# Performance work log

Hardware: AMD Instinct MI355X
Metric: run time of the kernel (lower is better)

The kernel has to match this reference:

```python
import jax, jax.numpy as jnp
import numpy as np

N, M_CTX, SIN, YDIM, SPROJ = 16384, 4096, 256, 7, 256


def setup_inputs() -> dict:
    key = jax.random.key(0)
    k1, k2, k3, k4, k5 = jax.random.split(key, 5)
    return {
        "x": jax.random.normal(k1, (N, SIN), dtype=jnp.float32),
        "y": jax.random.normal(k2, (M_CTX, YDIM), dtype=jnp.float32),
        "Wq": jax.random.normal(k3, (SIN, SPROJ), dtype=jnp.float32) / np.sqrt(SIN),
        "Wk": jax.random.normal(k4, (YDIM, SPROJ), dtype=jnp.float32) / np.sqrt(YDIM),
        "Wv": jax.random.normal(k5, (YDIM, SPROJ), dtype=jnp.float32) / np.sqrt(YDIM),
    }


def smooth_softmax(x):
    # softmax over keys (axis=1) blended with 0.1*relu, renormalized
    s = jax.nn.softmax(x, axis=1)
    num = jax.nn.relu(x) * 0.1 + s
    return num / jnp.sum(num, axis=1, keepdims=True)


def reference(x, y, Wq, Wk, Wv):
    XQ = x @ Wq            # [N, P]
    YK = y @ Wk            # [M, P]
    YV = y @ Wv            # [M, P]
    scores = (XQ @ YK.T) / jnp.sqrt(jnp.asarray(YK.shape[1], XQ.dtype))  # [N, M]
    A = smooth_softmax(scores)
    return A @ YV          # [N, P]
```

## Files before the change

### kernel.cpp

```cpp
#include <hip/hip_runtime.h>
#include <hip/hip_bf16.h>

#define N_Q   16384
#define MCTX  4096
#define DSIN  256
#define YDIM  7
#define PDIM  256
#define BK    32

typedef __attribute__((ext_vector_type(8))) short s16x8;
typedef __attribute__((ext_vector_type(4))) float f32x4;
typedef unsigned short u16;

static __device__ __forceinline__ u16 f2bf(float f) {
    union { float f; unsigned u; } v; v.f = f;
    unsigned r = v.u + 0x7fffu + ((v.u >> 16) & 1u);
    return (u16)(r >> 16);
}
static __device__ __forceinline__ float bf2f(u16 h) {
    union { unsigned u; float f; } v; v.u = ((unsigned)h) << 16;
    return v.f;
}
static __device__ __forceinline__ f32x4 mfma16(s16x8 a, s16x8 b, f32x4 c) {
    return __builtin_amdgcn_mfma_f32_16x16x32_bf16(a, b, c, 0, 0, 0);
}
static __device__ __forceinline__ void gload_lds16(const u16* g, u16* l) {
    __builtin_amdgcn_global_load_lds(
        (const __attribute__((address_space(1))) unsigned int*)(g),
        (__attribute__((address_space(3))) unsigned int*)(l), 16, 0, 0);
}

__global__ void k_wt(const float* __restrict__ Wq, u16* __restrict__ WtH,
                     u16* __restrict__ WtL) {
    int n = blockIdx.x;
    int k = threadIdx.x;
    float w = Wq[(size_t)k * PDIM + n];
    u16 h = f2bf(w);
    WtH[(size_t)n * DSIN + k] = h;
    WtL[(size_t)n * DSIN + k] = f2bf(w - bf2f(h));
}

__global__ void k_ykv(const float* __restrict__ y, const float* __restrict__ Wk,
                      const float* __restrict__ Wv, u16* __restrict__ YK,
                      u16* __restrict__ YVb) {
    int kb = blockIdx.x;
    int p  = threadIdx.x;
    float wk[YDIM], wv[YDIM];
#pragma unroll
    for (int j = 0; j < YDIM; ++j) {
        wk[j] = Wk[(size_t)j * PDIM + p];
        wv[j] = Wv[(size_t)j * PDIM + p];
    }
    u16 vbuf[32];
#pragma unroll
    for (int m = 0; m < 32; ++m) {
        int key = kb * 32 + m;
        float ak = 0.f, av = 0.f;
#pragma unroll
        for (int j = 0; j < YDIM; ++j) {
            float yy = y[(size_t)key * YDIM + j];
            ak += yy * wk[j];
            av += yy * wv[j];
        }
        YK[(size_t)key * PDIM + p] = f2bf(ak * 0.0625f);
        vbuf[m] = f2bf(av);
    }
    s16x8* dst = (s16x8*)(YVb + ((size_t)kb * PDIM + p) * 32);
#pragma unroll
    for (int c = 0; c < 4; ++c) dst[c] = ((s16x8*)vbuf)[c];
}

__global__ __launch_bounds__(256, 1) void k_xq(const float* __restrict__ x,
                                               const u16* __restrict__ WtH,
                                               const u16* __restrict__ WtL,
                                               u16* __restrict__ XQ) {
    __shared__ u16 xH[64 * 256];
    __shared__ u16 xL[64 * 256];
    const int tid = threadIdx.x;
    const int rowg0 = blockIdx.x * 64;

#pragma unroll
    for (int i = 0; i < 8; ++i) {
        int row = (tid >> 5) + i * 8;
        int c32 = tid & 31;
        const float* px = x + (size_t)(rowg0 + row) * DSIN + c32 * 8;
        float4 a = *(const float4*)px;
        float4 b = *(const float4*)(px + 4);
        float vals[8] = {a.x, a.y, a.z, a.w, b.x, b.y, b.z, b.w};
        s16x8 h, l;
#pragma unroll
        for (int j = 0; j < 8; ++j) {
            u16 hh = f2bf(vals[j]);
            h[j] = (short)hh;
            l[j] = (short)f2bf(vals[j] - bf2f(hh));
        }
        int pc = c32 ^ (row & 7);
        *(s16x8*)(xH + row * 256 + pc * 8) = h;
        *(s16x8*)(xL + row * 256 + pc * 8) = l;
    }
    __syncthreads();

    const int wave = tid >> 6, lane = tid & 63;
    const int quad = lane >> 4, m16 = lane & 15;
    const int rowl = wave * 16 + m16;
    const int swz = rowl & 7;
    s16x8 ah[8], al[8];
#pragma unroll
    for (int kf = 0; kf < 8; ++kf) {
        int pc = (kf * 4 + quad) ^ swz;
        ah[kf] = *(const s16x8*)(xH + rowl * 256 + pc * 8);
        al[kf] = *(const s16x8*)(xL + rowl * 256 + pc * 8);
    }
#pragma unroll
    for (int pt = 0; pt < 16; ++pt) {
        f32x4 acc = (f32x4){0.f, 0.f, 0.f, 0.f};
#pragma unroll
        for (int kf = 0; kf < 8; ++kf) {
            size_t idx = (size_t)(pt * 16 + m16) * DSIN + kf * 32 + quad * 8;
            s16x8 bh = *(const s16x8*)(WtH + idx);
            s16x8 bl = *(const s16x8*)(WtL + idx);
            acc = mfma16(ah[kf], bh, acc);
            acc = mfma16(al[kf], bh, acc);
            acc = mfma16(ah[kf], bl, acc);
        }
#pragma unroll
        for (int r = 0; r < 4; ++r)
            XQ[(size_t)(rowg0 + wave * 16 + quad * 4 + r) * PDIM + pt * 16 + m16] =
                f2bf(acc[r]);
    }
}

__global__ __launch_bounds__(256, 2) void k_attn(const u16* __restrict__ XQ,
                                                 const u16* __restrict__ YK,
                                                 const u16* __restrict__ YVb,
                                                 float* __restrict__ accE,
                                                 float* __restrict__ accR,
                                                 float* __restrict__ lsum,
                                                 float* __restrict__ rsum,
                                                 int msPerSplit) {
    __shared__ u16 Kt[32 * 256];
    __shared__ u16 Pe[64 * 40];
    __shared__ u16 Pr[64 * 40];

    const int tid = threadIdx.x;
    const int wave = tid >> 6, lane = tid & 63;
    const int quad = lane >> 4, m16 = lane & 15;
    const int split = blockIdx.y;
    const int qbase = blockIdx.x * 64;
    const int key_begin = split * msPerSplit;
    const int iters = msPerSplit / BK;
    const int pslice = wave * 64;
    const int swz = m16 & 7;

    s16x8 qf[8];
    const u16* qp = XQ + (size_t)(qbase + wave * 16 + m16) * DSIN;
#pragma unroll
    for (int kf = 0; kf < 8; ++kf)
        qf[kf] = *(const s16x8*)(qp + kf * 32 + quad * 8);

    f32x4 aE[4][4], aR[4][4];
#pragma unroll
    for (int g = 0; g < 4; ++g)
#pragma unroll
        for (int t = 0; t < 4; ++t) {
            aE[g][t] = (f32x4){0.f, 0.f, 0.f, 0.f};
            aR[g][t] = (f32x4){0.f, 0.f, 0.f, 0.f};
        }
    float lacc[4] = {0.f, 0.f, 0.f, 0.f}, racc[4] = {0.f, 0.f, 0.f, 0.f};

    auto stage = [&](int key0) {
#pragma unroll
        for (int c = 0; c < 4; ++c) {
            int l = (wave * 4 + c) * 64 + lane;
            int r = l >> 5;
            int sc = (l & 31) ^ (r & 7);
            gload_lds16(YK + (size_t)(key0 + r) * DSIN + sc * 8,
                        Kt + (size_t)(wave * 4 + c) * 512);
        }
    };
    stage(key_begin);

    for (int it = 0; it < iters; ++it) {
        const int key0 = key_begin + it * BK;
        __syncthreads();

        f32x4 s0 = (f32x4){0.f, 0.f, 0.f, 0.f};
        f32x4 s1 = (f32x4){0.f, 0.f, 0.f, 0.f};
#pragma unroll
        for (int kf = 0; kf < 8; ++kf) {
            int pc = (kf * 4 + quad) ^ swz;
            s16x8 b0 = *(const s16x8*)(Kt + m16 * 256 + pc * 8);
            s16x8 b1 = *(const s16x8*)(Kt + (16 + m16) * 256 + pc * 8);
            s0 = mfma16(qf[kf], b0, s0);
            s1 = mfma16(qf[kf], b1, s1);
        }
#pragma unroll
        for (int r = 0; r < 4; ++r) {
            float e0 = __expf(s0[r]), e1 = __expf(s1[r]);
            float rl0 = fmaxf(s0[r], 0.f), rl1 = fmaxf(s1[r], 0.f);
            lacc[r] += e0 + e1;
            racc[r] += rl0 + rl1;
            int row = wave * 16 + quad * 4 + r;
            Pe[row * 40 + m16]      = f2bf(e0);
            Pe[row * 40 + 16 + m16] = f2bf(e1);
            Pr[row * 40 + m16]      = f2bf(rl0);
            Pr[row * 40 + 16 + m16] = f2bf(rl1);
        }
        __syncthreads();

        s16x8 vf[4];
        const u16* vb = YVb + (size_t)((key0 >> 5) * PDIM) * 32;
#pragma unroll
        for (int t = 0; t < 4; ++t)
            vf[t] = *(const s16x8*)(vb + (size_t)(pslice + t * 16 + m16) * 32 + quad * 8);

        if (it + 1 < iters) stage(key0 + BK);

#pragma unroll
        for (int g = 0; g < 4; ++g) {
            s16x8 pa = *(const s16x8*)(Pe + (g * 16 + m16) * 40 + quad * 8);
            s16x8 pb = *(const s16x8*)(Pr + (g * 16 + m16) * 40 + quad * 8);
#pragma unroll
            for (int t = 0; t < 4; ++t) {
                aE[g][t] = mfma16(pa, vf[t], aE[g][t]);
                aR[g][t] = mfma16(pb, vf[t], aR[g][t]);
            }
        }
    }

    size_t ob = ((size_t)split * N_Q + qbase) * PDIM;
#pragma unroll
    for (int g = 0; g < 4; ++g)
#pragma unroll
        for (int t = 0; t < 4; ++t)
#pragma unroll
            for (int r = 0; r < 4; ++r) {
                size_t o = ob + (size_t)(g * 16 + quad * 4 + r) * PDIM + pslice + t * 16 + m16;
                accE[o] = aE[g][t][r];
                accR[o] = aR[g][t][r];
            }
#pragma unroll
    for (int r = 0; r < 4; ++r) {
        lacc[r] += __shfl_xor(lacc[r], 1);
        lacc[r] += __shfl_xor(lacc[r], 2);
        lacc[r] += __shfl_xor(lacc[r], 4);
        lacc[r] += __shfl_xor(lacc[r], 8);
        racc[r] += __shfl_xor(racc[r], 1);
        racc[r] += __shfl_xor(racc[r], 2);
        racc[r] += __shfl_xor(racc[r], 4);
        racc[r] += __shfl_xor(racc[r], 8);
    }
    if (m16 < 4) {
        float lv = (m16 == 0) ? lacc[0] : (m16 == 1) ? lacc[1] : (m16 == 2) ? lacc[2] : lacc[3];
        float rv = (m16 == 0) ? racc[0] : (m16 == 1) ? racc[1] : (m16 == 2) ? racc[2] : racc[3];
        int row = split * N_Q + qbase + wave * 16 + quad * 4 + m16;
        lsum[row] = lv;
        rsum[row] = rv;
    }
}

__global__ void k_comb(const float* __restrict__ accE, const float* __restrict__ accR,
                       const float* __restrict__ lsum, const float* __restrict__ rsum,
                       float* __restrict__ out, int nsplit) {
    int row = blockIdx.x * 4 + (threadIdx.x >> 6);
    size_t idx = (size_t)row * PDIM + (threadIdx.x & 63) * 4;
    const size_t NP = (size_t)N_Q * PDIM;
    float4 E = {0.f, 0.f, 0.f, 0.f}, R = {0.f, 0.f, 0.f, 0.f};
    float L = 0.f, Rs = 0.f;
    for (int s = 0; s < nsplit; ++s) {
        float4 e = *(const float4*)(accE + s * NP + idx);
        float4 r = *(const float4*)(accR + s * NP + idx);
        E.x += e.x; E.y += e.y; E.z += e.z; E.w += e.w;
        R.x += r.x; R.y += r.y; R.z += r.z; R.w += r.w;
        L  += lsum[(size_t)s * N_Q + row];
        Rs += rsum[(size_t)s * N_Q + row];
    }
    float invL = 1.f / L, invD = 1.f / (1.f + 0.1f * Rs);
    float4 o;
    o.x = (0.1f * R.x + E.x * invL) * invD;
    o.y = (0.1f * R.y + E.y * invL) * invD;
    o.z = (0.1f * R.z + E.z * invL) * invD;
    o.w = (0.1f * R.w + E.w * invL) * invD;
    *(float4*)(out + idx) = o;
}

extern "C" void kernel_launch(void* const* d_in, const int* in_sizes, int n_in,
                              void* d_out, int out_size, void* d_ws, size_t ws_size,
                              hipStream_t stream) {
    const float* x  = (const float*)d_in[0];
    const float* y  = (const float*)d_in[1];
    const float* Wq = (const float*)d_in[2];
    const float* Wk = (const float*)d_in[3];
    const float* Wv = (const float*)d_in[4];
    float* out = (float*)d_out;

    char* ws = (char*)d_ws;
    size_t off = 0;
    auto take = [&](size_t bytes) -> char* {
        char* p = ws + off;
        off += (bytes + 255) & ~(size_t)255;
        return p;
    };
    u16* XQ  = (u16*)take((size_t)N_Q * PDIM * 2);
    u16* WtH = (u16*)take((size_t)PDIM * DSIN * 2);
    u16* WtL = (u16*)take((size_t)PDIM * DSIN * 2);
    u16* YK  = (u16*)take((size_t)MCTX * PDIM * 2);
    u16* YVb = (u16*)take((size_t)MCTX * PDIM * 2);

    size_t perSplit = (size_t)N_Q * PDIM * 4 * 2 + (size_t)N_Q * 4 * 2 + 1024;
    int nsplit = (ws_size >= off + 2 * perSplit + 4096) ? 2 : 1;

    float* accE = (float*)take((size_t)nsplit * N_Q * PDIM * 4);
    float* accR = (float*)take((size_t)nsplit * N_Q * PDIM * 4);
    float* lsum = (float*)take((size_t)nsplit * N_Q * 4);
    float* rsum = (float*)take((size_t)nsplit * N_Q * 4);

    hipLaunchKernelGGL(k_wt,   dim3(PDIM),     dim3(DSIN), 0, stream, Wq, WtH, WtL);
    hipLaunchKernelGGL(k_ykv,  dim3(MCTX/32),  dim3(PDIM), 0, stream, y, Wk, Wv, YK, YVb);
    hipLaunchKernelGGL(k_xq,   dim3(N_Q/64),   dim3(256),  0, stream, x, WtH, WtL, XQ);
    hipLaunchKernelGGL(k_attn, dim3(N_Q/64, nsplit), dim3(256), 0, stream,
                       XQ, YK, YVb, accE, accR, lsum, rsum, MCTX / nsplit);
    hipLaunchKernelGGL(k_comb, dim3(N_Q/4),    dim3(256),  0, stream,
                       accE, accR, lsum, rsum, out, nsplit);
}
```

Measured before the change: 236.6 us.

## Shrink query tiles, split keys across waves, store bf16 partials, add setprio

Halves the query tile in k_xq and k_attn from 64 to 32 rows. In k_attn each wave now computes scores for one 16-key half of the block and the row sums are reduced through shared memory; occupancy hints are raised. The split-K partial accumulators are stored as bf16 instead of fp32, halving the write and read traffic in k_comb, at some cost in precision. s_setprio is wrapped around the MFMA sections to favour matrix issue. The smaller tile doubles the number of YK/YV loads per query row, trading reuse for parallelism and occupancy.

```diff
diff --git a/kernel.cpp b/kernel.cpp
--- a/kernel.cpp
+++ b/kernel.cpp
@@ -70,17 +70,17 @@
     for (int c = 0; c < 4; ++c) dst[c] = ((s16x8*)vbuf)[c];
 }
 
-__global__ __launch_bounds__(256, 1) void k_xq(const float* __restrict__ x,
+__global__ __launch_bounds__(256, 2) void k_xq(const float* __restrict__ x,
                                                const u16* __restrict__ WtH,
                                                const u16* __restrict__ WtL,
                                                u16* __restrict__ XQ) {
-    __shared__ u16 xH[64 * 256];
-    __shared__ u16 xL[64 * 256];
+    __shared__ u16 xH[32 * 256];
+    __shared__ u16 xL[32 * 256];
     const int tid = threadIdx.x;
-    const int rowg0 = blockIdx.x * 64;
-
-#pragma unroll
-    for (int i = 0; i < 8; ++i) {
+    const int rowg0 = blockIdx.x * 32;
+
+#pragma unroll
+    for (int i = 0; i < 4; ++i) {
         int row = (tid >> 5) + i * 8;
         int c32 = tid & 31;
         const float* px = x + (size_t)(rowg0 + row) * DSIN + c32 * 8;
@@ -102,7 +102,8 @@
 
     const int wave = tid >> 6, lane = tid & 63;
     const int quad = lane >> 4, m16 = lane & 15;
-    const int rowl = wave * 16 + m16;
+    const int rh = wave & 1, ph = wave >> 1;
+    const int rowl = rh * 16 + m16;
     const int swz = rowl & 7;
     s16x8 ah[8], al[8];
 #pragma unroll
@@ -112,7 +113,8 @@
         al[kf] = *(const s16x8*)(xL + rowl * 256 + pc * 8);
     }
 #pragma unroll
-    for (int pt = 0; pt < 16; ++pt) {
+    for (int ptl = 0; ptl < 8; ++ptl) {
+        int pt = ph * 8 + ptl;
         f32x4 acc = (f32x4){0.f, 0.f, 0.f, 0.f};
 #pragma unroll
         for (int kf = 0; kf < 8; ++kf) {
@@ -125,42 +127,45 @@
         }
 #pragma unroll
         for (int r = 0; r < 4; ++r)
-            XQ[(size_t)(rowg0 + wave * 16 + quad * 4 + r) * PDIM + pt * 16 + m16] =
+            XQ[(size_t)(rowg0 + rh * 16 + quad * 4 + r) * PDIM + pt * 16 + m16] =
                 f2bf(acc[r]);
     }
 }
 
-__global__ __launch_bounds__(256, 2) void k_attn(const u16* __restrict__ XQ,
+__global__ __launch_bounds__(256, 3) void k_attn(const u16* __restrict__ XQ,
                                                  const u16* __restrict__ YK,
                                                  const u16* __restrict__ YVb,
-                                                 float* __restrict__ accE,
-                                                 float* __restrict__ accR,
+                                                 u16* __restrict__ accE,
+                                                 u16* __restrict__ accR,
                                                  float* __restrict__ lsum,
                                                  float* __restrict__ rsum,
                                                  int msPerSplit) {
     __shared__ u16 Kt[32 * 256];
-    __shared__ u16 Pe[64 * 40];
-    __shared__ u16 Pr[64 * 40];
+    __shared__ u16 Pe[32 * 40];
+    __shared__ u16 Pr[32 * 40];
+    __shared__ float Lred[2][32];
+    __shared__ float Rred[2][32];
 
     const int tid = threadIdx.x;
     const int wave = tid >> 6, lane = tid & 63;
     const int quad = lane >> 4, m16 = lane & 15;
+    const int rh = wave >> 1, kh = wave & 1;
     const int split = blockIdx.y;
-    const int qbase = blockIdx.x * 64;
+    const int qbase = blockIdx.x * 32;
     const int key_begin = split * msPerSplit;
     const int iters = msPerSplit / BK;
     const int pslice = wave * 64;
     const int swz = m16 & 7;
 
     s16x8 qf[8];
-    const u16* qp = XQ + (size_t)(qbase + wave * 16 + m16) * DSIN;
+    const u16* qp = XQ + (size_t)(qbase + rh * 16 + m16) * DSIN;
 #pragma unroll
     for (int kf = 0; kf < 8; ++kf)
         qf[kf] = *(const s16x8*)(qp + kf * 32 + quad * 8);
 
-    f32x4 aE[4][4], aR[4][4];
-#pragma unroll
-    for (int g = 0; g < 4; ++g)
+    f32x4 aE[2][4], aR[2][4];
+#pragma unroll
+    for (int g = 0; g < 2; ++g)
 #pragma unroll
         for (int t = 0; t < 4; ++t) {
             aE[g][t] = (f32x4){0.f, 0.f, 0.f, 0.f};
@@ -185,26 +190,23 @@
         __syncthreads();
 
         f32x4 s0 = (f32x4){0.f, 0.f, 0.f, 0.f};
-        f32x4 s1 = (f32x4){0.f, 0.f, 0.f, 0.f};
+        __builtin_amdgcn_s_setprio(1);
 #pragma unroll
         for (int kf = 0; kf < 8; ++kf) {
             int pc = (kf * 4 + quad) ^ swz;
-            s16x8 b0 = *(const s16x8*)(Kt + m16 * 256 + pc * 8);
-            s16x8 b1 = *(const s16x8*)(Kt + (16 + m16) * 256 + pc * 8);
+            s16x8 b0 = *(const s16x8*)(Kt + (kh * 16 + m16) * 256 + pc * 8);
             s0 = mfma16(qf[kf], b0, s0);
-            s1 = mfma16(qf[kf], b1, s1);
-        }
+        }
+        __builtin_amdgcn_s_setprio(0);
 #pragma unroll
         for (int r = 0; r < 4; ++r) {
-            float e0 = __expf(s0[r]), e1 = __expf(s1[r]);
-            float rl0 = fmaxf(s0[r], 0.f), rl1 = fmaxf(s1[r], 0.f);
-            lacc[r] += e0 + e1;
-            racc[r] += rl0 + rl1;
-            int row = wave * 16 + quad * 4 + r;
-            Pe[row * 40 + m16]      = f2bf(e0);
-            Pe[row * 40 + 16 + m16] = f2bf(e1);
-            Pr[row * 40 + m16]      = f2bf(rl0);
-            Pr[row * 40 + 16 + m16] = f2bf(rl1);
+            float e0 = __expf(s0[r]);
+            float rl0 = fmaxf(s0[r], 0.f);
+            lacc[r] += e0;
+            racc[r] += rl0;
+            int row = rh * 16 + quad * 4 + r;
+            Pe[row * 40 + kh * 16 + m16] = f2bf(e0);
+            Pr[row * 40 + kh * 16 + m16] = f2bf(rl0);
         }
         __syncthreads();
 
@@ -216,8 +218,9 @@
 
         if (it + 1 < iters) stage(key0 + BK);
 
-#pragma unroll
-        for (int g = 0; g < 4; ++g) {
+        __builtin_amdgcn_s_setprio(1);
+#pragma unroll
+        for (int g = 0; g < 2; ++g) {
             s16x8 pa = *(const s16x8*)(Pe + (g * 16 + m16) * 40 + quad * 8);
             s16x8 pb = *(const s16x8*)(Pr + (g * 16 + m16) * 40 + quad * 8);
 #pragma unroll
@@ -226,18 +229,19 @@
                 aR[g][t] = mfma16(pb, vf[t], aR[g][t]);
             }
         }
+        __builtin_amdgcn_s_setprio(0);
     }
 
     size_t ob = ((size_t)split * N_Q + qbase) * PDIM;
 #pragma unroll
-    for (int g = 0; g < 4; ++g)
+    for (int g = 0; g < 2; ++g)
 #pragma unroll
         for (int t = 0; t < 4; ++t)
 #pragma unroll
             for (int r = 0; r < 4; ++r) {
                 size_t o = ob + (size_t)(g * 16 + quad * 4 + r) * PDIM + pslice + t * 16 + m16;
-                accE[o] = aE[g][t][r];
-                accR[o] = aR[g][t][r];
+                accE[o] = f2bf(aE[g][t][r]);
+                accR[o] = f2bf(aR[g][t][r]);
             }
 #pragma unroll
     for (int r = 0; r < 4; ++r) {
@@ -250,38 +254,54 @@
         racc[r] += __shfl_xor(racc[r], 4);
         racc[r] += __shfl_xor(racc[r], 8);
     }
-    if (m16 < 4) {
-        float lv = (m16 == 0) ? lacc[0] : (m16 == 1) ? lacc[1] : (m16 == 2) ? lacc[2] : lacc[3];
-        float rv = (m16 == 0) ? racc[0] : (m16 == 1) ? racc[1] : (m16 == 2) ? racc[2] : racc[3];
-        int row = split * N_Q + qbase + wave * 16 + quad * 4 + m16;
-        lsum[row] = lv;
-        rsum[row] = rv;
-    }
-}
-
-__global__ void k_comb(const float* __restrict__ accE, const float* __restrict__ accR,
+    if (m16 == 0) {
+#pragma unroll
+        for (int r = 0; r < 4; ++r) {
+            Lred[kh][rh * 16 + quad * 4 + r] = lacc[r];
+            Rred[kh][rh * 16 + quad * 4 + r] = racc[r];
+        }
+    }
+    __syncthreads();
+    if (tid < 32) {
+        int row = split * N_Q + qbase + tid;
+        lsum[row] = Lred[0][tid] + Lred[1][tid];
+        rsum[row] = Rred[0][tid] + Rred[1][tid];
+    }
+}
+
+__global__ void k_comb(const u16* __restrict__ accE, const u16* __restrict__ accR,
                        const float* __restrict__ lsum, const float* __restrict__ rsum,
                        float* __restrict__ out, int nsplit) {
-    int row = blockIdx.x * 4 + (threadIdx.x >> 6);
-    size_t idx = (size_t)row * PDIM + (threadIdx.x & 63) * 4;
+    int row = blockIdx.x * 8 + (threadIdx.x >> 5);
+    int col = (threadIdx.x & 31) * 8;
+    size_t idx = (size_t)row * PDIM + col;
     const size_t NP = (size_t)N_Q * PDIM;
-    float4 E = {0.f, 0.f, 0.f, 0.f}, R = {0.f, 0.f, 0.f, 0.f};
+    float E[8] = {0.f, 0.f, 0.f, 0.f, 0.f, 0.f, 0.f, 0.f};
+    float R[8] = {0.f, 0.f, 0.f, 0.f, 0.f, 0.f, 0.f, 0.f};
     float L = 0.f, Rs = 0.f;
     for (int s = 0; s < nsplit; ++s) {
-        float4 e = *(const float4*)(accE + s * NP + idx);
-        float4 r = *(const float4*)(accR + s * NP + idx);
-        E.x += e.x; E.y += e.y; E.z += e.z; E.w += e.w;
-        R.x += r.x; R.y += r.y; R.z += r.z; R.w += r.w;
+        s16x8 e = *(const s16x8*)(accE + s * NP + idx);
+        s16x8 r = *(const s16x8*)(accR + s * NP + idx);
+#pragma unroll
+        for (int j = 0; j < 8; ++j) {
+            E[j] += bf2f((u16)e[j]);
+            R[j] += bf2f((u16)r[j]);
+        }
         L  += lsum[(size_t)s * N_Q + row];
         Rs += rsum[(size_t)s * N_Q + row];
     }
     float invL = 1.f / L, invD = 1.f / (1.f + 0.1f * Rs);
-    float4 o;
-    o.x = (0.1f * R.x + E.x * invL) * invD;
-    o.y = (0.1f * R.y + E.y * invL) * invD;
-    o.z = (0.1f * R.z + E.z * invL) * invD;
-    o.w = (0.1f * R.w + E.w * invL) * invD;
-    *(float4*)(out + idx) = o;
+    float4 o0, o1;
+    o0.x = (0.1f * R[0] + E[0] * invL) * invD;
+    o0.y = (0.1f * R[1] + E[1] * invL) * invD;
+    o0.z = (0.1f * R[2] + E[2] * invL) * invD;
+    o0.w = (0.1f * R[3] + E[3] * invL) * invD;
+    o1.x = (0.1f * R[4] + E[4] * invL) * invD;
+    o1.y = (0.1f * R[5] + E[5] * invL) * invD;
+    o1.z = (0.1f * R[6] + E[6] * invL) * invD;
+    o1.w = (0.1f * R[7] + E[7] * invL) * invD;
+    *(float4*)(out + idx) = o0;
+    *(float4*)(out + idx + 4) = o1;
 }
 
 extern "C" void kernel_launch(void* const* d_in, const int* in_sizes, int n_in,
@@ -307,19 +327,19 @@
     u16* YK  = (u16*)take((size_t)MCTX * PDIM * 2);
     u16* YVb = (u16*)take((size_t)MCTX * PDIM * 2);
 
-    size_t perSplit = (size_t)N_Q * PDIM * 4 * 2 + (size_t)N_Q * 4 * 2 + 1024;
+    size_t perSplit = (size_t)N_Q * PDIM * 2 * 2 + (size_t)N_Q * 4 * 2 + 1024;
     int nsplit = (ws_size >= off + 2 * perSplit + 4096) ? 2 : 1;
 
-    float* accE = (float*)take((size_t)nsplit * N_Q * PDIM * 4);
-    float* accR = (float*)take((size_t)nsplit * N_Q * PDIM * 4);
+    u16*   accE = (u16*)take((size_t)nsplit * N_Q * PDIM * 2);
+    u16*   accR = (u16*)take((size_t)nsplit * N_Q * PDIM * 2);
     float* lsum = (float*)take((size_t)nsplit * N_Q * 4);
     float* rsum = (float*)take((size_t)nsplit * N_Q * 4);
 
     hipLaunchKernelGGL(k_wt,   dim3(PDIM),     dim3(DSIN), 0, stream, Wq, WtH, WtL);
     hipLaunchKernelGGL(k_ykv,  dim3(MCTX/32),  dim3(PDIM), 0, stream, y, Wk, Wv, YK, YVb);
-    hipLaunchKernelGGL(k_xq,   dim3(N_Q/64),   dim3(256),  0, stream, x, WtH, WtL, XQ);
-    hipLaunchKernelGGL(k_attn, dim3(N_Q/64, nsplit), dim3(256), 0, stream,
+    hipLaunchKernelGGL(k_xq,   dim3(N_Q/32),   dim3(256),  0, stream, x, WtH, WtL, XQ);
+    hipLaunchKernelGGL(k_attn, dim3(N_Q/32, nsplit), dim3(256), 0, stream,
                        XQ, YK, YVb, accE, accR, lsum, rsum, MCTX / nsplit);
-    hipLaunchKernelGGL(k_comb, dim3(N_Q/4),    dim3(256),  0, stream,
+    hipLaunchKernelGGL(k_comb, dim3(N_Q/8),    dim3(256),  0, stream,
                        accE, accR, lsum, rsum, out, nsplit);
 }
```

Result: slower. 354.7 us (+49.9%).
